# Kernel tuning notes

Measured on AMD Instinct MI355X. Metric: run time of the kernel, lower is better.

Reference implementation:

```python
import jax, jax.numpy as jnp
import numpy as np

B, L, HS = 2, 2048, 2048
NH, NKV, HD = 16, 4, 128
EPS = 1e-6
ROPE_BASE = 10000.0
SCALE = HD ** -0.5


def setup_inputs() -> dict:
    key = jax.random.key(0)
    ks = jax.random.split(key, 5)
    w = lambda k, shape: (jax.random.normal(k, shape, jnp.float32) * 0.02)
    return {
        "hidden_states": jax.random.normal(ks[0], (B, L, HS), jnp.float32),
        "Wq": w(ks[1], (HS, NH * HD)),
        "Wk": w(ks[2], (HS, NKV * HD)),
        "Wv": w(ks[3], (HS, NKV * HD)),
        "Wo": w(ks[4], (NH * HD, HS)),
        "q_norm_w": jnp.ones((HD,), jnp.float32),
        "k_norm_w": jnp.ones((HD,), jnp.float32),
    }


def _rmsnorm(x, w):
    return x * jax.lax.rsqrt(jnp.mean(x * x, axis=-1, keepdims=True) + EPS) * w


def _rope(x, cos, sin):
    # x: [B, L, heads, HD]; cos/sin: [1, L, 1, HD//2]
    x1, x2 = jnp.split(x, 2, axis=-1)
    return jnp.concatenate([x1 * cos - x2 * sin, x2 * cos + x1 * sin], axis=-1)


def reference(hidden_states, Wq, Wk, Wv, Wo, q_norm_w, k_norm_w):
    b, l, _ = hidden_states.shape
    n_rep = NH // NKV
    q = (hidden_states @ Wq).reshape(b, l, NH, HD)
    k = (hidden_states @ Wk).reshape(b, l, NKV, HD)
    v = (hidden_states @ Wv).reshape(b, l, NKV, HD)
    # QK RMSNorm over head_dim
    q = _rmsnorm(q, q_norm_w)
    k = _rmsnorm(k, k_norm_w)
    # RoPE with position_ids = arange(L)
    pos = jnp.arange(l, dtype=jnp.float32)
    inv_freq = 1.0 / (ROPE_BASE ** (jnp.arange(0, HD, 2, dtype=jnp.float32) / HD))
    ang = pos[:, None] * inv_freq  # [L, HD//2]
    cos = jnp.cos(ang)[None, :, None, :]
    sin = jnp.sin(ang)[None, :, None, :]
    q = _rope(q, cos, sin)
    k = _rope(k, cos, sin)
    # GQA: torch expand+reshape gives q head h -> kv head (h mod NKV);
    # reshape q to [B, L, n_rep, NKV, HD] (h = r*NKV + j) and contract per kv group.
    qg = q.reshape(b, l, n_rep, NKV, HD)
    scores = jnp.einsum("blrjd,bmjd->brjlm", qg, k) * SCALE  # [B, r, j, L, L]
    causal = jnp.tril(jnp.ones((l, l), dtype=bool))
    scores = jnp.where(causal, scores, -jnp.inf)
    probs = jax.nn.softmax(scores, axis=-1)
    out = jnp.einsum("brjlm,bmjd->blrjd", probs, v).reshape(b, l, NH * HD)
    return out @ Wo
```

## Files before the change

### kernel.cpp

```cpp
#include <hip/hip_runtime.h>
#include <hip/hip_bf16.h>

#define B_  2
#define L_  2048
#define HS_ 2048
#define NH_ 16
#define NKV_ 4
#define HD_ 128
#define EPS_ 1e-6f
#define SCALE_ 0.08838834764831843f
#define LOG2E_ 1.4426950408889634f

typedef __attribute__((ext_vector_type(8))) short bf16x8;
typedef __attribute__((ext_vector_type(4))) float f32x4;

__device__ __forceinline__ f32x4 mfma16(bf16x8 a, bf16x8 b, f32x4 c) {
    return __builtin_amdgcn_mfma_f32_16x16x32_bf16(a, b, c, 0, 0, 0);
}

__device__ __forceinline__ void async_copy16(void* lds, const void* g) {
    __builtin_amdgcn_global_load_lds(
        (const __attribute__((address_space(1))) unsigned int*)g,
        (__attribute__((address_space(3))) unsigned int*)lds,
        16, 0, 0);
}

__device__ __forceinline__ unsigned cvtpk(float lo, float hi) {
    unsigned r;
    asm("v_cvt_pk_bf16_f32 %0, %1, %2" : "=v"(r) : "v"(lo), "v"(hi));
    return r;
}

__global__ __launch_bounds__(256) void cvt_f32_bf16(const float* __restrict__ src,
                                                    __hip_bfloat16* __restrict__ dst,
                                                    int n4) {
    int i = blockIdx.x * 256 + threadIdx.x;
    if (i >= n4) return;
    float4 v = ((const float4*)src)[i];
    union { __hip_bfloat16 h[4]; short4 s; } u;
    u.h[0] = __float2bfloat16(v.x);
    u.h[1] = __float2bfloat16(v.y);
    u.h[2] = __float2bfloat16(v.z);
    u.h[3] = __float2bfloat16(v.w);
    ((short4*)dst)[i] = u.s;
}

__global__ __launch_bounds__(256) void transpose_cvt(const float* __restrict__ src,
                                                     __hip_bfloat16* __restrict__ dst,
                                                     int K, int N) {
    __shared__ float tile[32][33];
    int n0 = blockIdx.x * 32, k0 = blockIdx.y * 32;
    int tx = threadIdx.x & 31, ty = threadIdx.x >> 5;
#pragma unroll
    for (int i = 0; i < 32; i += 8)
        tile[ty + i][tx] = src[(size_t)(k0 + ty + i) * N + n0 + tx];
    __syncthreads();
#pragma unroll
    for (int i = 0; i < 32; i += 8)
        dst[(size_t)(n0 + ty + i) * K + k0 + tx] = __float2bfloat16(tile[tx][ty + i]);
}

__global__ __launch_bounds__(256) void v_transpose(const float* __restrict__ KV,
                                                   __hip_bfloat16* __restrict__ Vt) {
    __shared__ float tile[32][33];
    int bkv = blockIdx.z;
    int b = bkv >> 2, kv = bkv & 3;
    int l0 = blockIdx.x * 32, d0 = blockIdx.y * 32;
    int tx = threadIdx.x & 31, ty = threadIdx.x >> 5;
#pragma unroll
    for (int i = 0; i < 32; i += 8)
        tile[ty + i][tx] = KV[(size_t)(b * L_ + l0 + ty + i) * 1024 + 512 + kv * HD_ + d0 + tx];
    __syncthreads();
#pragma unroll
    for (int i = 0; i < 32; i += 8)
        Vt[((size_t)(b * NKV_ + kv) * HD_ + d0 + ty + i) * L_ + l0 + tx] =
            __float2bfloat16(tile[tx][ty + i]);
}

#define BM 128
#define BN 128
#define BKK 64
__global__ __launch_bounds__(256, 2) void gemm_bf16(const __hip_bfloat16* __restrict__ A,
                                                    const __hip_bfloat16* __restrict__ Bt,
                                                    float* __restrict__ C,
                                                    int M, int N, int K) {
    __shared__ __align__(16) __hip_bfloat16 sA[BM * BKK];
    __shared__ __align__(16) __hip_bfloat16 sB[BN * BKK];
    int t = threadIdx.x;
    int wave = t >> 6, lane = t & 63;
    int row16 = lane & 15, quad = lane >> 4;
    int m0 = blockIdx.x * BM, n0 = blockIdx.y * BN;
    int waveM = (wave >> 1) * 64, waveN = (wave & 1) * 64;
    f32x4 acc[4][4] = {};

    for (int k0 = 0; k0 < K; k0 += BKK) {
#pragma unroll
        for (int i = 0; i < 4; ++i) {
            int c = i * 256 + t;
            int r = c >> 3, kc = (c & 7) * 8;
            async_copy16(&sA[c * 8], A + (size_t)(m0 + r) * K + k0 + kc);
            async_copy16(&sB[c * 8], Bt + (size_t)(n0 + r) * K + k0 + kc);
        }
        __syncthreads();
#pragma unroll
        for (int kc = 0; kc < 2; ++kc) {
            bf16x8 a[4], b[4];
#pragma unroll
            for (int i = 0; i < 4; ++i)
                a[i] = *(const bf16x8*)&sA[(waveM + i * 16 + row16) * BKK + kc * 32 + quad * 8];
#pragma unroll
            for (int j = 0; j < 4; ++j)
                b[j] = *(const bf16x8*)&sB[(waveN + j * 16 + row16) * BKK + kc * 32 + quad * 8];
#pragma unroll
            for (int i = 0; i < 4; ++i)
#pragma unroll
                for (int j = 0; j < 4; ++j)
                    acc[i][j] = mfma16(a[i], b[j], acc[i][j]);
        }
        __syncthreads();
    }
#pragma unroll
    for (int i = 0; i < 4; ++i)
#pragma unroll
        for (int j = 0; j < 4; ++j) {
            int rbase = m0 + waveM + i * 16 + quad * 4;
            int col = n0 + waveN + j * 16 + row16;
#pragma unroll
            for (int r = 0; r < 4; ++r)
                C[(size_t)(rbase + r) * N + col] = acc[i][j][r];
        }
}

#define GNT 32
#define GKB 4096
__global__ __launch_bounds__(512, 2) void gemm8_bf16(const __hip_bfloat16* __restrict__ A,
                                                     const __hip_bfloat16* __restrict__ Bt,
                                                     float* __restrict__ C1,
                                                     float* __restrict__ C2,
                                                     int Ntot, int splitN) {
    __shared__ __align__(16) char lds[131072];
    int t = threadIdx.x;
    int w = t >> 6, lane = t & 63;
    int row16 = lane & 15, quad = lane >> 4, e7 = row16 & 7;
    int wr = w >> 2, wc = w & 3;

    int gx = gridDim.x;
    int nwg = gx * gridDim.y;
    int bid = blockIdx.y * gx + blockIdx.x;
    int cpx = nwg >> 3;
    int swz = (bid & 7) * cpx + (bid >> 3);
    int bx = swz % gx, by = swz / gx;
    int m0 = bx * 256, n0 = by * 256;

    const char* baseA[2];
    const char* baseB[2];
#pragma unroll
    for (int kc = 0; kc < 2; ++kc) {
        int so = ((kc * 4 + quad) ^ e7) << 4;
        baseA[kc] = lds + wr * 16384 + row16 * 128 + so;
        baseB[kc] = lds + 65536 + wc * 8192 + row16 * 128 + so;
    }

    int r8 = lane >> 3;
    int sl = (lane & 7) ^ r8;
    char* dstA = lds + wr * 16384 + (w & 3) * 2048 + lane * 16;
    char* dstB = lds + 65536 + (w >> 1) * 8192 + (w & 1) * 2048 + lane * 16;
    const char* gA = (const char*)A +
        (size_t)(m0 + wr * 128 + (w & 3) * 16 + r8) * GKB + sl * 16;
    const char* gB = (const char*)Bt +
        (size_t)(n0 + (w >> 1) * 64 + (w & 1) * 16 + r8) * GKB + sl * 16;

    f32x4 acc[8][4] = {};
    bf16x8 a[4][2], b[2][2];

#pragma unroll
    for (int i = 0; i < 2; ++i) async_copy16(dstA + i * 1024, gA + i * 32768);
#pragma unroll
    for (int i = 0; i < 2; ++i) async_copy16(dstB + i * 1024, gB + i * 32768);
#pragma unroll
    for (int i = 0; i < 2; ++i) async_copy16(dstB + 4096 + i * 1024, gB + 131072 + i * 32768);
#pragma unroll
    for (int i = 0; i < 2; ++i) async_copy16(dstA + 8192 + i * 1024, gA + 262144 + i * 32768);

    for (int Tb = 0; Tb < GNT; Tb += 2) {
#pragma unroll
        for (int u = 0; u < 2; ++u) {
            const int T = Tb + u;
            const int cu = u * 32768, du = (u ^ 1) * 32768;
            const int tn = (T + 1 < GNT ? T + 1 : T) * 128;

            asm volatile("s_waitcnt vmcnt(4)" ::: "memory");
            __builtin_amdgcn_s_barrier();
            __builtin_amdgcn_sched_barrier(0);
#pragma unroll
            for (int mi = 0; mi < 4; ++mi)
#pragma unroll
                for (int kc = 0; kc < 2; ++kc)
                    a[mi][kc] = *(const bf16x8*)(baseA[kc] + cu + mi * 2048);
#pragma unroll
            for (int ni = 0; ni < 2; ++ni)
#pragma unroll
                for (int kc = 0; kc < 2; ++kc)
                    b[ni][kc] = *(const bf16x8*)(baseB[kc] + cu + ni * 2048);
#pragma unroll
            for (int i = 0; i < 2; ++i)
                async_copy16(dstA + du + i * 1024, gA + tn + i * 32768);
            asm volatile("s_waitcnt lgkmcnt(0)" ::: "memory");
            __builtin_amdgcn_sched_barrier(0);
            __builtin_amdgcn_s_setprio(1);
#pragma unroll
            for (int mi = 0; mi < 4; ++mi)
#pragma unroll
                for (int ni = 0; ni < 2; ++ni)
#pragma unroll
                    for (int kc = 0; kc < 2; ++kc)
                        acc[mi][ni] = mfma16(a[mi][kc], b[ni][kc], acc[mi][ni]);
            __builtin_amdgcn_s_setprio(0);

            asm volatile("s_waitcnt vmcnt(4)" ::: "memory");
            __builtin_amdgcn_s_barrier();
            __builtin_amdgcn_sched_barrier(0);
#pragma unroll
            for (int ni = 0; ni < 2; ++ni)
#pragma unroll
                for (int kc = 0; kc < 2; ++kc)
                    b[ni][kc] = *(const bf16x8*)(baseB[kc] + cu + 4096 + ni * 2048);
#pragma unroll
            for (int i = 0; i < 2; ++i)
                async_copy16(dstB + du + i * 1024, gB + tn + i * 32768);
            asm volatile("s_waitcnt lgkmcnt(0)" ::: "memory");
            __builtin_amdgcn_sched_barrier(0);
            __builtin_amdgcn_s_setprio(1);
#pragma unroll
            for (int mi = 0; mi < 4; ++mi)
#pragma unroll
                for (int ni = 0; ni < 2; ++ni)
#pragma unroll
                    for (int kc = 0; kc < 2; ++kc)
                        acc[mi][2 + ni] = mfma16(a[mi][kc], b[ni][kc], acc[mi][2 + ni]);
            __builtin_amdgcn_s_setprio(0);

            asm volatile("s_waitcnt vmcnt(4)" ::: "memory");
            __builtin_amdgcn_s_barrier();
            __builtin_amdgcn_sched_barrier(0);
#pragma unroll
            for (int mi = 0; mi < 4; ++mi)
#pragma unroll
                for (int kc = 0; kc < 2; ++kc)
                    a[mi][kc] = *(const bf16x8*)(baseA[kc] + cu + 8192 + mi * 2048);
#pragma unroll
            for (int i = 0; i < 2; ++i)
                async_copy16(dstB + du + 4096 + i * 1024, gB + 131072 + tn + i * 32768);
            asm volatile("s_waitcnt lgkmcnt(0)" ::: "memory");
            __builtin_amdgcn_sched_barrier(0);
            __builtin_amdgcn_s_setprio(1);
#pragma unroll
            for (int mi = 0; mi < 4; ++mi)
#pragma unroll
                for (int ni = 0; ni < 2; ++ni)
#pragma unroll
                    for (int kc = 0; kc < 2; ++kc)
                        acc[4 + mi][2 + ni] = mfma16(a[mi][kc], b[ni][kc], acc[4 + mi][2 + ni]);
            __builtin_amdgcn_s_setprio(0);

            __builtin_amdgcn_s_barrier();
            __builtin_amdgcn_sched_barrier(0);
#pragma unroll
            for (int ni = 0; ni < 2; ++ni)
#pragma unroll
                for (int kc = 0; kc < 2; ++kc)
                    b[ni][kc] = *(const bf16x8*)(baseB[kc] + cu + ni * 2048);
#pragma unroll
            for (int i = 0; i < 2; ++i)
                async_copy16(dstA + du + 8192 + i * 1024, gA + 262144 + tn + i * 32768);
            asm volatile("s_waitcnt lgkmcnt(0)" ::: "memory");
            __builtin_amdgcn_sched_barrier(0);
            __builtin_amdgcn_s_setprio(1);
#pragma unroll
            for (int mi = 0; mi < 4; ++mi)
#pragma unroll
                for (int ni = 0; ni < 2; ++ni)
#pragma unroll
                    for (int kc = 0; kc < 2; ++kc)
                        acc[4 + mi][ni] = mfma16(a[mi][kc], b[ni][kc], acc[4 + mi][ni]);
            __builtin_amdgcn_s_setprio(0);
        }
    }

    float* Cb; int cs, ccol0;
    if (n0 < splitN) { Cb = C1; cs = splitN; ccol0 = n0; }
    else             { Cb = C2; cs = Ntot - splitN; ccol0 = n0 - splitN; }
#pragma unroll
    for (int mi = 0; mi < 8; ++mi)
#pragma unroll
        for (int ni = 0; ni < 4; ++ni) {
            int rbase = m0 + wr * 128 + mi * 16 + quad * 4;
            int col = ccol0 + wc * 64 + ni * 16 + row16;
#pragma unroll
            for (int r = 0; r < 4; ++r)
                Cb[(size_t)(rbase + r) * cs + col] = acc[mi][ni][r];
        }
}

__global__ __launch_bounds__(256) void norm_rope(const float* __restrict__ X,
                                                 __hip_bfloat16* __restrict__ Y,
                                                 const float* __restrict__ w,
                                                 int log2nh, int in_stride, float oscale) {
    int row = blockIdx.x * 4 + (threadIdx.x >> 6);
    int lane = threadIdx.x & 63;
    int m = row >> log2nh;
    int head = row & ((1 << log2nh) - 1);
    int pos = m & (L_ - 1);
    const float* x = X + (size_t)m * in_stride + head * HD_;
    float x1 = x[lane], x2 = x[lane + 64];
    float ss = x1 * x1 + x2 * x2;
#pragma unroll
    for (int mm = 1; mm < 64; mm <<= 1) ss += __shfl_xor(ss, mm);
    float rms = rsqrtf(ss * (1.0f / 128.0f) + EPS_);
    float xn1 = x1 * rms * w[lane];
    float xn2 = x2 * rms * w[lane + 64];
    float inv_freq = __builtin_exp2f(-(float)lane * 0.20762050593046014f);
    float ang = (float)pos * inv_freq;
    float c = cosf(ang), s = sinf(ang);
    __hip_bfloat16* y = Y + (size_t)row * HD_;
    y[lane]      = __float2bfloat16((xn1 * c - xn2 * s) * oscale);
    y[lane + 64] = __float2bfloat16((xn2 * c + xn1 * s) * oscale);
}

__global__ __launch_bounds__(256, 2) void flash_attn(const __hip_bfloat16* __restrict__ Q,
                                                     const __hip_bfloat16* __restrict__ Kb,
                                                     const __hip_bfloat16* __restrict__ Vt,
                                                     __hip_bfloat16* __restrict__ O) {
    __shared__ __align__(16) __hip_bfloat16 sK[2][64 * 128];
    __shared__ __align__(16) __hip_bfloat16 sV[2][128 * 64];
    __shared__ __align__(16) __hip_bfloat16 sP[4][16 * 72];

    int t = threadIdx.x, wave = t >> 6, lane = t & 63;
    int row16 = lane & 15, quad = lane >> 4;
    int h = blockIdx.y, b = blockIdx.z;
    int kv = h & (NKV_ - 1);
    int x = blockIdx.x;
    int qtA = x, qtB = 31 - x;
    int nA = qtA + 1;
    const int nTot = 33;

    int e7 = row16 & 7;
    int kOff[4], vOff[2];
#pragma unroll
    for (int kc = 0; kc < 4; ++kc)
        kOff[kc] = row16 * 256 + (((kc * 4 + quad) ^ e7) * 16);
#pragma unroll
    for (int kc2 = 0; kc2 < 2; ++kc2)
        vOff[kc2] = row16 * 128 + (((kc2 * 4 + quad) ^ e7) * 16);

    const char* sKb = (const char*)&sK[0][0];
    const char* sVb = (const char*)&sV[0][0];
    char* myP = (char*)&sP[wave][0];
    int pW = row16 * 144 + quad * 8;
    int pR = row16 * 144 + quad * 16;

    const char* gK[4];
    const char* gV[4];
#pragma unroll
    for (int i = 0; i < 4; ++i) {
        int rk = wave * 16 + i * 4 + quad;
        int ck = row16 ^ (rk & 7);
        gK[i] = (const char*)(Kb + ((size_t)(b * L_ + rk) * NKV_ + kv) * HD_ + ck * 8);
        int rv = wave * 32 + i * 8 + (lane >> 3);
        int cv = (lane & 7) ^ (rv & 7);
        gV[i] = (const char*)(Vt + ((size_t)(b * NKV_ + kv) * HD_ + rv) * L_ + cv * 8);
    }
    char* dK = (char*)&sK[0][0] + wave * 4096 + lane * 16;
    char* dV = (char*)&sV[0][0] + wave * 4096 + lane * 16;

    bf16x8 qf[4];
    f32x4 accO[8];
    float lrow;
    int q0w = 0;

    auto loadQ = [&](int qt) {
        q0w = qt * 64 + wave * 16;
        const __hip_bfloat16* qbase =
            Q + ((size_t)(b * L_ + q0w + row16) * NH_ + h) * HD_ + quad * 8;
#pragma unroll
        for (int kc = 0; kc < 4; ++kc) qf[kc] = *(const bf16x8*)(qbase + kc * 32);
#pragma unroll
        for (int db = 0; db < 8; ++db) accO[db] = f32x4{0.f, 0.f, 0.f, 0.f};
        lrow = 0.f;
    };

    auto epilogue = [&]() {
        float l = lrow;
        l += __shfl_xor(l, 16);
        l += __shfl_xor(l, 32);
        float linv = 1.0f / l;
        __hip_bfloat16* obase = O + ((size_t)(b * L_ + q0w + row16) * NH_ + h) * HD_;
#pragma unroll
        for (int db = 0; db < 8; ++db) {
            union { __hip_bfloat16 h4[4]; short4 s4; } u;
#pragma unroll
            for (int r = 0; r < 4; ++r) u.h4[r] = __float2bfloat16(accO[db][r] * linv);
            *(short4*)(obase + db * 16 + quad * 4) = u.s4;
        }
    };

    auto stage = [&](int s1) {
        int kb64 = (s1 < nA ? s1 : s1 - nA) * 64;
        int buf = (s1 & 1) * 16384;
        int ko = kb64 * 1024;
        int vo = kb64 * 2;
#pragma unroll
        for (int i = 0; i < 4; ++i) {
            async_copy16(dK + buf + i * 1024, gK[i] + ko);
            async_copy16(dV + buf + i * 1024, gV[i] + vo);
        }
    };

    loadQ(qtA);
    stage(0);
    for (int s = 0; s < nTot; ++s) {
        __syncthreads();
        if (s + 1 < nTot) stage(s + 1);
        if (s == nA) { epilogue(); loadQ(qtB); }
        int kcur = (s < nA ? s : s - nA) * 64;
        const char* cK = sKb + (s & 1) * 16384;
        const char* cV = sVb + (s & 1) * 16384;

        f32x4 st[4];
        __builtin_amdgcn_s_setprio(1);
#pragma unroll
        for (int kb = 0; kb < 4; ++kb) {
            f32x4 acc = {};
#pragma unroll
            for (int kc = 0; kc < 4; ++kc) {
                bf16x8 kf = *(const bf16x8*)(cK + kb * 4096 + kOff[kc]);
                acc = mfma16(kf, qf[kc], acc);
            }
            st[kb] = acc;
        }
        __builtin_amdgcn_s_setprio(0);

        float p[4][4];
        if (kcur + 63 > q0w) {
            int qgRel = q0w + row16 - kcur - quad * 4;
#pragma unroll
            for (int kb = 0; kb < 4; ++kb)
#pragma unroll
                for (int r = 0; r < 4; ++r) {
                    float e = __builtin_exp2f(st[kb][r]);
                    p[kb][r] = (kb * 16 + r <= qgRel) ? e : 0.f;
                }
        } else {
#pragma unroll
            for (int kb = 0; kb < 4; ++kb)
#pragma unroll
                for (int r = 0; r < 4; ++r)
                    p[kb][r] = __builtin_exp2f(st[kb][r]);
        }
#pragma unroll
        for (int kb = 0; kb < 4; ++kb)
#pragma unroll
            for (int r = 0; r < 4; ++r) lrow += p[kb][r];

#pragma unroll
        for (int kb = 0; kb < 4; ++kb) {
            uint2 u;
            u.x = cvtpk(p[kb][0], p[kb][1]);
            u.y = cvtpk(p[kb][2], p[kb][3]);
            *(uint2*)(myP + pW + kb * 32) = u;
        }
        asm volatile("s_waitcnt lgkmcnt(0)" ::: "memory");
        bf16x8 pf[2];
        pf[0] = *(const bf16x8*)(myP + pR);
        pf[1] = *(const bf16x8*)(myP + pR + 64);

        __builtin_amdgcn_s_setprio(1);
#pragma unroll
        for (int db = 0; db < 8; ++db) {
#pragma unroll
            for (int kc2 = 0; kc2 < 2; ++kc2) {
                bf16x8 vf = *(const bf16x8*)(cV + db * 2048 + vOff[kc2]);
                accO[db] = mfma16(vf, pf[kc2], accO[db]);
            }
        }
        __builtin_amdgcn_s_setprio(0);
    }
    epilogue();
}

extern "C" void kernel_launch(void* const* d_in, const int* in_sizes, int n_in,
                              void* d_out, int out_size, void* d_ws, size_t ws_size,
                              hipStream_t stream) {
    const float* hidden = (const float*)d_in[0];
    const float* Wq = (const float*)d_in[1];
    const float* Wk = (const float*)d_in[2];
    const float* Wv = (const float*)d_in[3];
    const float* Wo = (const float*)d_in[4];
    const float* qw = (const float*)d_in[5];
    const float* kw = (const float*)d_in[6];
    float* out = (float*)d_out;

    char* ws = (char*)d_ws;
    size_t off = 0;
    auto alloc = [&](size_t bytes) { char* p = ws + off; off += (bytes + 255) & ~255ull; return p; };
    __hip_bfloat16* Wq_t = (__hip_bfloat16*)alloc((size_t)HS_ * NH_ * HD_ * 2);
    __hip_bfloat16* Wk_t = (__hip_bfloat16*)alloc((size_t)HS_ * NKV_ * HD_ * 2);
    __hip_bfloat16* Wv_t = (__hip_bfloat16*)alloc((size_t)HS_ * NKV_ * HD_ * 2);
    __hip_bfloat16* Wo_t = (__hip_bfloat16*)alloc((size_t)HS_ * NH_ * HD_ * 2);
    __hip_bfloat16* A_h  = (__hip_bfloat16*)alloc((size_t)B_ * L_ * HS_ * 2);
    float* kv_f32 = (float*)alloc((size_t)B_ * L_ * 1024 * 4);
    __hip_bfloat16* q_bf  = (__hip_bfloat16*)alloc((size_t)B_ * L_ * NH_ * HD_ * 2);
    __hip_bfloat16* k_bf  = (__hip_bfloat16*)alloc((size_t)B_ * L_ * NKV_ * HD_ * 2);
    __hip_bfloat16* vt_bf = (__hip_bfloat16*)alloc((size_t)B_ * NKV_ * HD_ * L_ * 2);
    float* q_f32 = out;
    __hip_bfloat16* attn_bf = A_h;

    const int M = B_ * L_;

    cvt_f32_bf16<<<(M * HS_ / 4 + 255) / 256, 256, 0, stream>>>(hidden, A_h, M * HS_ / 4);
    transpose_cvt<<<dim3(2048 / 32, 2048 / 32), 256, 0, stream>>>(Wq, Wq_t, HS_, 2048);
    transpose_cvt<<<dim3(512 / 32, 2048 / 32), 256, 0, stream>>>(Wk, Wk_t, HS_, 512);
    transpose_cvt<<<dim3(512 / 32, 2048 / 32), 256, 0, stream>>>(Wv, Wv_t, HS_, 512);
    transpose_cvt<<<dim3(2048 / 32, 2048 / 32), 256, 0, stream>>>(Wo, Wo_t, HS_, 2048);
    gemm8_bf16<<<dim3(M / 256, 3072 / 256), 512, 0, stream>>>(
        A_h, Wq_t, q_f32, kv_f32, 3072, 2048);
    norm_rope<<<(M * NH_) / 4, 256, 0, stream>>>(q_f32, q_bf, qw, 4, 2048, SCALE_ * LOG2E_);
    norm_rope<<<(M * NKV_) / 4, 256, 0, stream>>>(kv_f32, k_bf, kw, 2, 1024, 1.0f);
    v_transpose<<<dim3(L_ / 32, HD_ / 32, B_ * NKV_), 256, 0, stream>>>(kv_f32, vt_bf);
    flash_attn<<<dim3(16, NH_, B_), 256, 0, stream>>>(q_bf, k_bf, vt_bf, attn_bf);
    gemm_bf16<<<dim3(M / BM, 2048 / BN), 256, 0, stream>>>(attn_bf, Wo_t, out, M, 2048, HS_);
}
```

Before: 318.7 us.

## Replace output-projection GEMM with pipelined swizzled 128x256 MFMA kernel

Replaces the simple 128x128 output-projection GEMM, which loads a tile, waits at a barrier and then computes, with a 512-thread 128x256-tile kernel. The new kernel double-buffers LDS, issues async global-to-LDS loads for the next K-step between MFMA phases, XOR-swizzles LDS to avoid bank conflicts, remaps workgroups for L2 locality, and raises wave priority around MFMA bursts. The aim is to hide memory latency and remove the idle time at each barrier. It costs more LDS and registers, and the hand-written waitcnt and barrier schedule is fragile.

Result: faster. 303.7 us (-4.7%).

```diff
diff --git a/kernel.cpp b/kernel.cpp
--- a/kernel.cpp
+++ b/kernel.cpp
@@ -77,60 +77,6 @@
             __float2bfloat16(tile[tx][ty + i]);
 }
 
-#define BM 128
-#define BN 128
-#define BKK 64
-__global__ __launch_bounds__(256, 2) void gemm_bf16(const __hip_bfloat16* __restrict__ A,
-                                                    const __hip_bfloat16* __restrict__ Bt,
-                                                    float* __restrict__ C,
-                                                    int M, int N, int K) {
-    __shared__ __align__(16) __hip_bfloat16 sA[BM * BKK];
-    __shared__ __align__(16) __hip_bfloat16 sB[BN * BKK];
-    int t = threadIdx.x;
-    int wave = t >> 6, lane = t & 63;
-    int row16 = lane & 15, quad = lane >> 4;
-    int m0 = blockIdx.x * BM, n0 = blockIdx.y * BN;
-    int waveM = (wave >> 1) * 64, waveN = (wave & 1) * 64;
-    f32x4 acc[4][4] = {};
-
-    for (int k0 = 0; k0 < K; k0 += BKK) {
-#pragma unroll
-        for (int i = 0; i < 4; ++i) {
-            int c = i * 256 + t;
-            int r = c >> 3, kc = (c & 7) * 8;
-            async_copy16(&sA[c * 8], A + (size_t)(m0 + r) * K + k0 + kc);
-            async_copy16(&sB[c * 8], Bt + (size_t)(n0 + r) * K + k0 + kc);
-        }
-        __syncthreads();
-#pragma unroll
-        for (int kc = 0; kc < 2; ++kc) {
-            bf16x8 a[4], b[4];
-#pragma unroll
-            for (int i = 0; i < 4; ++i)
-                a[i] = *(const bf16x8*)&sA[(waveM + i * 16 + row16) * BKK + kc * 32 + quad * 8];
-#pragma unroll
-            for (int j = 0; j < 4; ++j)
-                b[j] = *(const bf16x8*)&sB[(waveN + j * 16 + row16) * BKK + kc * 32 + quad * 8];
-#pragma unroll
-            for (int i = 0; i < 4; ++i)
-#pragma unroll
-                for (int j = 0; j < 4; ++j)
-                    acc[i][j] = mfma16(a[i], b[j], acc[i][j]);
-        }
-        __syncthreads();
-    }
-#pragma unroll
-    for (int i = 0; i < 4; ++i)
-#pragma unroll
-        for (int j = 0; j < 4; ++j) {
-            int rbase = m0 + waveM + i * 16 + quad * 4;
-            int col = n0 + waveN + j * 16 + row16;
-#pragma unroll
-            for (int r = 0; r < 4; ++r)
-                C[(size_t)(rbase + r) * N + col] = acc[i][j][r];
-        }
-}
-
 #define GNT 32
 #define GKB 4096
 __global__ __launch_bounds__(512, 2) void gemm8_bf16(const __hip_bfloat16* __restrict__ A,
@@ -299,6 +245,171 @@
 #pragma unroll
             for (int r = 0; r < 4; ++r)
                 Cb[(size_t)(rbase + r) * cs + col] = acc[mi][ni][r];
+        }
+}
+
+__global__ __launch_bounds__(512, 2) void gemm_o(const __hip_bfloat16* __restrict__ A,
+                                                 const __hip_bfloat16* __restrict__ Bt,
+                                                 float* __restrict__ C) {
+    __shared__ __align__(16) char lds[98304];
+    int t = threadIdx.x;
+    int w = t >> 6, lane = t & 63;
+    int row16 = lane & 15, quad = lane >> 4, e7 = row16 & 15 & 7;
+    int wr = w >> 2, wc = w & 3;
+
+    int gx = gridDim.x;
+    int nwg = gx * gridDim.y;
+    int bid = blockIdx.y * gx + blockIdx.x;
+    int cpx = nwg >> 3;
+    int swz = (bid & 7) * cpx + (bid >> 3);
+    int bx = swz % gx, by = swz / gx;
+    int m0 = bx * 128, n0 = by * 256;
+
+    const char* baseA[2];
+    const char* baseB[2];
+#pragma unroll
+    for (int kc = 0; kc < 2; ++kc) {
+        int so = ((kc * 4 + quad) ^ e7) << 4;
+        baseA[kc] = lds + wr * 8192 + row16 * 128 + so;
+        baseB[kc] = lds + 32768 + wc * 8192 + row16 * 128 + so;
+    }
+
+    int r8 = lane >> 3;
+    int sl = (lane & 7) ^ r8;
+    int arow_lo = ((w & 4) << 4) + (w & 3) * 8;
+    int li0 = w * 2;
+    int brow_lo0 = ((li0) >> 2) * 64 + ((li0) & 3) * 8;
+    int brow_lo1 = ((li0 + 1) >> 2) * 64 + ((li0 + 1) & 3) * 8;
+
+    char* dAlo = lds + arow_lo * 128 + lane * 16;
+    char* dBlo0 = lds + 32768 + brow_lo0 * 128 + lane * 16;
+    char* dBlo1 = lds + 32768 + brow_lo1 * 128 + lane * 16;
+    const char* gAlo = (const char*)A + (size_t)(m0 + arow_lo + r8) * GKB + sl * 16;
+    const char* gBlo0 = (const char*)Bt + (size_t)(n0 + brow_lo0 + r8) * GKB + sl * 16;
+    const char* gBlo1 = (const char*)Bt + (size_t)(n0 + brow_lo1 + r8) * GKB + sl * 16;
+    const int HI_L = 32 * 128;
+    const size_t HI_G = (size_t)32 * GKB;
+
+    f32x4 acc[4][4] = {};
+    bf16x8 a[2][2], b[2][2];
+
+    async_copy16(dAlo, gAlo);
+    async_copy16(dBlo0, gBlo0);
+    async_copy16(dBlo1, gBlo1);
+    async_copy16(dBlo0 + HI_L, gBlo0 + HI_G);
+    async_copy16(dBlo1 + HI_L, gBlo1 + HI_G);
+    async_copy16(dAlo + HI_L, gAlo + HI_G);
+
+    for (int Tb = 0; Tb < GNT; Tb += 2) {
+#pragma unroll
+        for (int u = 0; u < 2; ++u) {
+            const int T = Tb + u;
+            const int cuA = u * 16384, duA = (u ^ 1) * 16384;
+            const int cuB = u * 32768, duB = (u ^ 1) * 32768;
+            const int tn = (T + 1 < GNT ? T + 1 : T) * 128;
+
+            asm volatile("s_waitcnt vmcnt(3)" ::: "memory");
+            __builtin_amdgcn_s_barrier();
+            __builtin_amdgcn_sched_barrier(0);
+#pragma unroll
+            for (int mi = 0; mi < 2; ++mi)
+#pragma unroll
+                for (int kc = 0; kc < 2; ++kc)
+                    a[mi][kc] = *(const bf16x8*)(baseA[kc] + cuA + mi * 2048);
+#pragma unroll
+            for (int ni = 0; ni < 2; ++ni)
+#pragma unroll
+                for (int kc = 0; kc < 2; ++kc)
+                    b[ni][kc] = *(const bf16x8*)(baseB[kc] + cuB + ni * 2048);
+            async_copy16(dAlo + duA, gAlo + tn);
+            asm volatile("s_waitcnt lgkmcnt(0)" ::: "memory");
+            __builtin_amdgcn_sched_barrier(0);
+            __builtin_amdgcn_s_setprio(1);
+#pragma unroll
+            for (int mi = 0; mi < 2; ++mi)
+#pragma unroll
+                for (int ni = 0; ni < 2; ++ni)
+#pragma unroll
+                    for (int kc = 0; kc < 2; ++kc)
+                        acc[mi][ni] = mfma16(a[mi][kc], b[ni][kc], acc[mi][ni]);
+            __builtin_amdgcn_s_setprio(0);
+
+            asm volatile("s_waitcnt vmcnt(2)" ::: "memory");
+            __builtin_amdgcn_s_barrier();
+            __builtin_amdgcn_sched_barrier(0);
+#pragma unroll
+            for (int ni = 0; ni < 2; ++ni)
+#pragma unroll
+                for (int kc = 0; kc < 2; ++kc)
+                    b[ni][kc] = *(const bf16x8*)(baseB[kc] + cuB + 4096 + ni * 2048);
+            async_copy16(dBlo0 + duB, gBlo0 + tn);
+            async_copy16(dBlo1 + duB, gBlo1 + tn);
+            asm volatile("s_waitcnt lgkmcnt(0)" ::: "memory");
+            __builtin_amdgcn_sched_barrier(0);
+            __builtin_amdgcn_s_setprio(1);
+#pragma unroll
+            for (int mi = 0; mi < 2; ++mi)
+#pragma unroll
+                for (int ni = 0; ni < 2; ++ni)
+#pragma unroll
+                    for (int kc = 0; kc < 2; ++kc)
+                        acc[mi][2 + ni] = mfma16(a[mi][kc], b[ni][kc], acc[mi][2 + ni]);
+            __builtin_amdgcn_s_setprio(0);
+
+            asm volatile("s_waitcnt vmcnt(3)" ::: "memory");
+            __builtin_amdgcn_s_barrier();
+            __builtin_amdgcn_sched_barrier(0);
+#pragma unroll
+            for (int mi = 0; mi < 2; ++mi)
+#pragma unroll
+                for (int kc = 0; kc < 2; ++kc)
+                    a[mi][kc] = *(const bf16x8*)(baseA[kc] + cuA + 4096 + mi * 2048);
+            async_copy16(dBlo0 + HI_L + duB, gBlo0 + HI_G + tn);
+            async_copy16(dBlo1 + HI_L + duB, gBlo1 + HI_G + tn);
+            asm volatile("s_waitcnt lgkmcnt(0)" ::: "memory");
+            __builtin_amdgcn_sched_barrier(0);
+            __builtin_amdgcn_s_setprio(1);
+#pragma unroll
+            for (int mi = 0; mi < 2; ++mi)
+#pragma unroll
+                for (int ni = 0; ni < 2; ++ni)
+#pragma unroll
+                    for (int kc = 0; kc < 2; ++kc)
+                        acc[2 + mi][2 + ni] = mfma16(a[mi][kc], b[ni][kc], acc[2 + mi][2 + ni]);
+            __builtin_amdgcn_s_setprio(0);
+
+            __builtin_amdgcn_s_barrier();
+            __builtin_amdgcn_sched_barrier(0);
+#pragma unroll
+            for (int ni = 0; ni < 2; ++ni)
+#pragma unroll
+                for (int kc = 0; kc < 2; ++kc)
+                    b[ni][kc] = *(const bf16x8*)(baseB[kc] + cuB + ni * 2048);
+            async_copy16(dAlo + HI_L + duA, gAlo + HI_G + tn);
+            asm volatile("s_waitcnt lgkmcnt(0)" ::: "memory");
+            __builtin_amdgcn_sched_barrier(0);
+            __builtin_amdgcn_s_setprio(1);
+#pragma unroll
+            for (int mi = 0; mi < 2; ++mi)
+#pragma unroll
+                for (int ni = 0; ni < 2; ++ni)
+#pragma unroll
+                    for (int kc = 0; kc < 2; ++kc)
+                        acc[2 + mi][ni] = mfma16(a[mi][kc], b[ni][kc], acc[2 + mi][ni]);
+            __builtin_amdgcn_s_setprio(0);
+        }
+    }
+    asm volatile("s_waitcnt vmcnt(0)" ::: "memory");
+
+#pragma unroll
+    for (int mi = 0; mi < 4; ++mi)
+#pragma unroll
+        for (int ni = 0; ni < 4; ++ni) {
+            int rbase = m0 + wr * 64 + mi * 16 + quad * 4;
+            int col = n0 + wc * 64 + ni * 16 + row16;
+#pragma unroll
+            for (int r = 0; r < 4; ++r)
+                C[(size_t)(rbase + r) * 2048 + col] = acc[mi][ni][r];
         }
 }
 
@@ -528,5 +639,5 @@
     norm_rope<<<(M * NKV_) / 4, 256, 0, stream>>>(kv_f32, k_bf, kw, 2, 1024, 1.0f);
     v_transpose<<<dim3(L_ / 32, HD_ / 32, B_ * NKV_), 256, 0, stream>>>(kv_f32, vt_bf);
     flash_attn<<<dim3(16, NH_, B_), 256, 0, stream>>>(q_bf, k_bf, vt_bf, attn_bf);
-    gemm_bf16<<<dim3(M / BM, 2048 / BN), 256, 0, stream>>>(attn_bf, Wo_t, out, M, 2048, HS_);
-}
+    gemm_o<<<dim3(M / 128, 2048 / 256), 512, 0, stream>>>(attn_bf, Wo_t, out);
+}
```
